# Performance work log

Measured on AMD Instinct MI355X. Metric: run time of the kernel, lower is better.

Reference implementation:

```python
import jax, jax.numpy as jnp
import numpy as np

B, N = 32, 200000          # images, flattened candidates per image (anchors*classes)
NUM_CLASSES = 21           # VOC-style class count for the label-offset trick
CONF_THR = 0.05            # cfg.PRED_CONF_THR
NMS_THR = 0.5              # cfg.PRED_NMS_THR
TOPK = 500                 # cfg.PRED_SELECT_TOPK
KEEP_MAX = 100             # cfg.PRED_NMS_KEEP


def setup_inputs() -> dict:
    key = jax.random.key(0)
    k1, k2, k3, k4 = jax.random.split(key, 4)
    pscores = jax.random.uniform(k1, (B, N), dtype=jnp.float32)
    # well-formed ltrb boxes in [0,1]: right>left, bottom>top
    xy1 = jax.random.uniform(k2, (B, N, 2), dtype=jnp.float32) * 0.8
    wh = jax.random.uniform(k3, (B, N, 2), dtype=jnp.float32) * 0.2 + 0.01
    pboxes = jnp.concatenate([xy1, xy1 + wh], axis=-1)
    plabels = jax.random.randint(k4, (B, N), 0, NUM_CLASSES)
    return {"pscores": pscores, "pboxes": pboxes, "plabels": plabels}


def _box_iou(a, b):
    # a: [K,4], b: [K,4] ltrb -> [K,K] pairwise IoU (torchvision convention)
    lt = jnp.maximum(a[:, None, :2], b[None, :, :2])
    rb = jnp.minimum(a[:, None, 2:], b[None, :, 2:])
    wh = jnp.clip(rb - lt, 0.0)
    inter = wh[..., 0] * wh[..., 1]
    area_a = (a[:, 2] - a[:, 0]) * (a[:, 3] - a[:, 1])
    area_b = (b[:, 2] - b[:, 0]) * (b[:, 3] - b[:, 1])
    return inter / (area_a[:, None] + area_b[None, :] - inter)


def _greedy_nms(iou_mat, valid, thr):
    # candidates are pre-sorted by score descending (lax.top_k output order)
    K = valid.shape[0]
    idxs = jnp.arange(K)

    def body(keep, i):
        suppressed = jnp.any(keep & (iou_mat[i] > thr) & (idxs < i))
        k = valid[i] & (~suppressed)
        return keep.at[i].set(k), None

    keep, _ = jax.lax.scan(body, jnp.zeros((K,), dtype=bool), idxs)
    return keep


def reference(pscores, pboxes, plabels):
    # ---- threshold + top-k pre-selection (mask_pos AND mask_topk) ----
    scores_k, idx = jax.lax.top_k(pscores, TOPK)          # [B,K] sorted desc
    valid = scores_k > CONF_THR                           # equivalent to mask_pos & mask_topk
    bidx = jnp.arange(B)[:, None]
    boxes_k = pboxes[bidx, idx]                           # [B,K,4]
    labels_k = plabels[bidx, idx]                         # [B,K]

    # ---- multi-class NMS via label offset trick (batched_nms) ----
    max_coord = jnp.max(jnp.where(valid[..., None], boxes_k, 0.0), axis=(1, 2))  # [B]
    offsets = labels_k.astype(boxes_k.dtype) * (max_coord[:, None] + 1.0)
    boxes_nms = boxes_k + offsets[..., None]              # [B,K,4]

    iou = jax.vmap(_box_iou)(boxes_nms, boxes_nms)        # [B,K,K]
    keep = jax.vmap(lambda m, v: _greedy_nms(m, v, NMS_THR))(iou, valid)  # [B,K] bool

    # ---- keep[:num_max] per batch ----
    rank = jnp.cumsum(keep.astype(jnp.int32), axis=1)
    keep = keep & (rank <= KEEP_MAX)

    # compact kept entries to front (jnp.argsort is stable -> score order preserved), pad to KEEP_MAX
    order = jnp.argsort(jnp.where(keep, 0, 1), axis=1)[:, :KEEP_MAX]       # [B,KEEP]
    out_valid = jnp.take_along_axis(keep, order, axis=1)                    # [B,KEEP]
    boxes2 = jnp.take_along_axis(boxes_k, order[..., None], axis=1) * out_valid[..., None]
    scores2 = jnp.take_along_axis(scores_k, order, axis=1) * out_valid
    labels2 = jnp.where(out_valid, jnp.take_along_axis(labels_k, order, axis=1), -1)
    ids_batch2 = jnp.where(out_valid, jnp.arange(B)[:, None], -1)
    return ids_batch2, boxes2, labels2, scores2, out_valid
```

## Files before the change

kernel.cpp:

```cpp
#include <hip/hip_runtime.h>
#include <stdint.h>

#pragma clang fp contract(off)

#define BB 32
#define NN 200000
#define N4 50000
#define KK 500
#define KEEPN 100
#define CONF 0.05f
#define NMSTHR 0.5f
#define SLICES 8
#define SLICE_F4 6250
#define LBINS 8192
#define LSHIFT 19
#define LOCAL_CAP 2048
#define OUT_CAP 576
#define M_CAP (SLICES * OUT_CAP)

typedef unsigned long long u64;


__device__ __forceinline__ unsigned int ordkey(float s) {
    unsigned int u = __float_as_uint(s);
    return (u & 0x80000000u) ? ~u : (u | 0x80000000u);
}

__global__ __launch_bounds__(1024) void select_kernel(const float4* __restrict__ ps4,
                                                      u64* __restrict__ cand,
                                                      unsigned int* __restrict__ cnts) {
    __shared__ unsigned int hist[LBINS];
    __shared__ u64 keys[LOCAL_CAP];
    __shared__ unsigned int h[256];
    __shared__ unsigned int wsum[16];
    __shared__ u64 s_prefix;
    __shared__ unsigned int s_t13, s_region, s_cntgt;
    __shared__ int s_lcnt, s_sc;

    const int b = blockIdx.y, x = blockIdx.x;
    const int tid = threadIdx.x, lane = tid & 63, wv = tid >> 6;
    const float4* p = ps4 + (size_t)b * N4 + (size_t)x * SLICE_F4;

    for (int i = tid; i < LBINS; i += 1024) hist[i] = 0;
    __syncthreads();
    for (int i = tid; i < SLICE_F4; i += 1024) {
        float4 v = p[i];
        atomicAdd(&hist[ordkey(v.x) >> LSHIFT], 1u);
        atomicAdd(&hist[ordkey(v.y) >> LSHIFT], 1u);
        atomicAdd(&hist[ordkey(v.z) >> LSHIFT], 1u);
        atomicAdd(&hist[ordkey(v.w) >> LSHIFT], 1u);
    }
    __syncthreads();

    unsigned int v8[8], tot = 0;
    for (int j = 0; j < 8; ++j) { v8[j] = hist[tid * 8 + j]; tot += v8[j]; }
    unsigned int sfx = tot;
    for (int off = 1; off < 64; off <<= 1) {
        unsigned int t2 = __shfl_down(sfx, off);
        sfx += (lane + off < 64) ? t2 : 0u;
    }
    if (lane == 0) wsum[wv] = sfx;
    __syncthreads();
    unsigned int wafter = 0;
    for (int w2 = wv + 1; w2 < 16; ++w2) wafter += wsum[w2];
    unsigned int sn = wafter + (sfx - tot);
    for (int j = 7; j >= 0; --j) {
        unsigned int s = sn + v8[j];
        if (s >= (unsigned)KK && sn < (unsigned)KK) s_t13 = (unsigned)(tid * 8 + j);
        sn = s;
    }
    if (tid == 0) s_lcnt = 0;
    __syncthreads();

    const unsigned int t13 = s_t13;
    const int ebase = x * (SLICE_F4 * 4);
    for (int i = tid; i < SLICE_F4; i += 1024) {
        float4 v = p[i];
        int n = ebase + (i << 2);
        unsigned int u;
        u = ordkey(v.x); if ((u >> LSHIFT) >= t13) { int pos = atomicAdd(&s_lcnt, 1);
            if (pos < LOCAL_CAP) keys[pos] = ((u64)u << 32) | (unsigned int)(~(unsigned int)(n)); }
        u = ordkey(v.y); if ((u >> LSHIFT) >= t13) { int pos = atomicAdd(&s_lcnt, 1);
            if (pos < LOCAL_CAP) keys[pos] = ((u64)u << 32) | (unsigned int)(~(unsigned int)(n + 1)); }
        u = ordkey(v.z); if ((u >> LSHIFT) >= t13) { int pos = atomicAdd(&s_lcnt, 1);
            if (pos < LOCAL_CAP) keys[pos] = ((u64)u << 32) | (unsigned int)(~(unsigned int)(n + 2)); }
        u = ordkey(v.w); if ((u >> LSHIFT) >= t13) { int pos = atomicAdd(&s_lcnt, 1);
            if (pos < LOCAL_CAP) keys[pos] = ((u64)u << 32) | (unsigned int)(~(unsigned int)(n + 3)); }
    }
    __syncthreads();
    int m = s_lcnt; if (m > LOCAL_CAP) m = LOCAL_CAP;

    u64 thr; int seln;
    if (m <= OUT_CAP) {
        thr = 0ULL; seln = m;
    } else {
        if (tid == 0) { s_prefix = 0ULL; s_cntgt = 0u; }
        __syncthreads();
        int shift = 56;
        for (; shift >= 0; shift -= 8) {
            if (tid < 256) h[tid] = 0u;
            __syncthreads();
            u64 pref = s_prefix;
            unsigned int cg = s_cntgt;
            for (int i = tid; i < m; i += 1024) {
                u64 k = keys[i];
                bool match = (shift == 56) || ((k >> (shift + 8)) == pref);
                if (match) atomicAdd(&h[(unsigned int)((k >> shift) & 0xFF)], 1u);
            }
            __syncthreads();
            if (wv == 0) {
                unsigned int b4[4]; unsigned int lt = 0;
                for (int j = 0; j < 4; ++j) { b4[j] = h[lane * 4 + j]; lt += b4[j]; }
                unsigned int sx = lt;
                for (int off = 1; off < 64; off <<= 1) {
                    unsigned int t2 = __shfl_down(sx, off);
                    sx += (lane + off < 64) ? t2 : 0u;
                }
                unsigned int after = sx - lt;
                unsigned int target = (unsigned)KK - cg;
                unsigned int sn2 = after;
                for (int j = 3; j >= 0; --j) {
                    unsigned int s = sn2 + b4[j];
                    if (s >= target && sn2 < target) {
                        unsigned int bin = (unsigned)(lane * 4 + j);
                        s_region = b4[j];
                        s_cntgt = cg + sn2;
                        s_prefix = (shift == 56) ? (u64)bin : ((pref << 8) | (u64)bin);
                    }
                    sn2 = s;
                }
            }
            __syncthreads();
            if (s_cntgt + s_region <= (unsigned)OUT_CAP) break;
        }
        if (shift < 0) shift = 0;
        thr = s_prefix << shift;
        seln = (int)(s_cntgt + s_region);
    }
    (void)seln;

    if (tid == 0) s_sc = 0;
    __syncthreads();
    u64* outslice = cand + (size_t)(b * SLICES + x) * OUT_CAP;
    for (int r0 = 0; r0 < LOCAL_CAP / 1024; ++r0) {
        int i = tid + r0 * 1024;
        u64 k = (i < m) ? keys[i] : 0ULL;
        bool pq = (i < m) && (k >= thr);
        u64 mb = __ballot(pq);
        int pre = __popcll(mb & ((1ULL << lane) - 1ULL));
        int tt = __popcll(mb);
        int base = 0;
        if (lane == 0 && tt > 0) base = atomicAdd(&s_sc, tt);
        base = __shfl(base, 0);
        if (pq && base + pre < OUT_CAP) outslice[base + pre] = k;
    }
    __syncthreads();
    if (tid == 0) {
        int c = s_sc; if (c > OUT_CAP) c = OUT_CAP;
        cnts[b * SLICES + x] = (unsigned)c;
    }
}

__global__ __launch_bounds__(1024) void final_kernel(const float* __restrict__ pboxes,
                                                     const int* __restrict__ plabels,
                                                     const u64* __restrict__ cand,
                                                     const unsigned int* __restrict__ cnts,
                                                     float* __restrict__ out) {
    __shared__ u64 kbuf[M_CAP];
    __shared__ u64 sel[OUT_CAP];
    __shared__ float sboxes[KK * 4];
    __shared__ float sscore[KK];
    __shared__ int slabel[KK];
    __shared__ int clist[KK];
    __shared__ unsigned int h[256];
    __shared__ int ccnt[21], coff[22], cfill[21];
    __shared__ u64 validw[8];
    __shared__ int kept[KEEPN];
    __shared__ float wred[16];
    __shared__ int soff[SLICES + 1];
    __shared__ u64 s_prefix;
    __shared__ unsigned int s_region, s_cntgt;
    __shared__ int s_sc, s_nk;
    __shared__ float s_maxc;

    const int b = blockIdx.x;
    const int tid = threadIdx.x;
    const int lane = tid & 63;
    const int wv = tid >> 6;

    if (tid == 0) {
        int acc = 0;
        for (int s = 0; s < SLICES; ++s) {
            soff[s] = acc;
            int c = (int)cnts[b * SLICES + s];
            if (c > OUT_CAP) c = OUT_CAP;
            acc += c;
        }
        soff[SLICES] = acc;
    }
    __syncthreads();
    int m = soff[SLICES];
    for (int s = 0; s < SLICES; ++s) {
        int off = soff[s], len = soff[s + 1] - off;
        const u64* src = cand + (size_t)(b * SLICES + s) * OUT_CAP;
        for (int i = tid; i < len; i += 1024) kbuf[off + i] = src[i];
    }
    __syncthreads();

    u64 thr; int seln;
    if (m <= OUT_CAP) {
        thr = 0ULL; seln = m;
    } else {
        if (tid == 0) { s_prefix = 0ULL; s_cntgt = 0u; }
        __syncthreads();
        int shift = 56;
        for (; shift >= 0; shift -= 8) {
            if (tid < 256) h[tid] = 0u;
            __syncthreads();
            u64 pref = s_prefix;
            unsigned int cg = s_cntgt;
            for (int i = tid; i < m; i += 1024) {
                u64 k = kbuf[i];
                bool match = (shift == 56) || ((k >> (shift + 8)) == pref);
                if (match) atomicAdd(&h[(unsigned int)((k >> shift) & 0xFF)], 1u);
            }
            __syncthreads();
            if (wv == 0) {
                unsigned int b4[4]; unsigned int lt = 0;
                for (int j = 0; j < 4; ++j) { b4[j] = h[lane * 4 + j]; lt += b4[j]; }
                unsigned int sx = lt;
                for (int off = 1; off < 64; off <<= 1) {
                    unsigned int t2 = __shfl_down(sx, off);
                    sx += (lane + off < 64) ? t2 : 0u;
                }
                unsigned int after = sx - lt;
                unsigned int target = (unsigned)KK - cg;
                unsigned int sn2 = after;
                for (int j = 3; j >= 0; --j) {
                    unsigned int s = sn2 + b4[j];
                    if (s >= target && sn2 < target) {
                        unsigned int bin = (unsigned)(lane * 4 + j);
                        s_region = b4[j];
                        s_cntgt = cg + sn2;
                        s_prefix = (shift == 56) ? (u64)bin : ((pref << 8) | (u64)bin);
                    }
                    sn2 = s;
                }
            }
            __syncthreads();
            if (s_cntgt + s_region <= (unsigned)OUT_CAP) break;
        }
        if (shift < 0) shift = 0;
        thr = s_prefix << shift;
        seln = (int)(s_cntgt + s_region);
    }

    if (tid == 0) s_sc = 0;
    __syncthreads();
    for (int r0 = 0; r0 < (M_CAP + 1023) / 1024; ++r0) {
        int i = tid + r0 * 1024;
        u64 k = (i < m) ? kbuf[i] : 0ULL;
        bool pq = (i < m) && (k >= thr);
        u64 mb = __ballot(pq);
        int pre = __popcll(mb & ((1ULL << lane) - 1ULL));
        int tt = __popcll(mb);
        int base = 0;
        if (lane == 0 && tt > 0) base = atomicAdd(&s_sc, tt);
        base = __shfl(base, 0);
        if (pq) sel[base + pre] = k;
    }
    __syncthreads();

    u64 myk = (tid < seln) ? sel[tid] : 0ULL;
    int r = 0;
    if ((tid & ~63) < seln) {
        for (int base = 0; base < seln; base += 64) {
            int i2 = base + lane;
            u64 other = (i2 < seln) ? sel[i2] : 0ULL;
            unsigned int olo = (unsigned int)other, ohi = (unsigned int)(other >> 32);
            int lim = seln - base; if (lim > 64) lim = 64;
            for (int t2 = 0; t2 < lim; ++t2) {
                unsigned int blo = (unsigned int)__builtin_amdgcn_readlane((int)olo, t2);
                unsigned int bhi = (unsigned int)__builtin_amdgcn_readlane((int)ohi, t2);
                u64 o = ((u64)bhi << 32) | (u64)blo;
                r += (o > myk) ? 1 : 0;
            }
        }
    }
    __syncthreads();
    if (tid < seln && r < KK) sel[r] = myk;
    __syncthreads();

    float sc = -1.0f;
    if (tid < KK) {
        u64 key = sel[tid];
        unsigned int lo = (unsigned int)key;
        unsigned int hi = (unsigned int)(key >> 32);
        int idx = (int)(~lo);
        unsigned int bits = (hi & 0x80000000u) ? (hi & 0x7FFFFFFFu) : ~hi;
        sc = __uint_as_float(bits);
        sscore[tid] = sc;
        const float4 bx = *(const float4*)(pboxes + (((size_t)b * NN + (size_t)idx) << 2));
        sboxes[tid * 4 + 0] = bx.x; sboxes[tid * 4 + 1] = bx.y;
        sboxes[tid * 4 + 2] = bx.z; sboxes[tid * 4 + 3] = bx.w;
        slabel[tid] = plabels[(size_t)b * NN + idx];
    }
    __syncthreads();

    bool vq = (tid < KK) && (sc > CONF);
    u64 bm = __ballot(vq);
    if (lane == 0 && wv < 8) validw[wv] = bm;
    float lm = vq ? fmaxf(fmaxf(sboxes[tid * 4 + 0], sboxes[tid * 4 + 1]),
                          fmaxf(sboxes[tid * 4 + 2], sboxes[tid * 4 + 3])) : 0.0f;
    for (int off = 32; off > 0; off >>= 1) lm = fmaxf(lm, __shfl_down(lm, off));
    if (lane == 0) wred[wv] = lm;
    __syncthreads();
    if (tid < 64) {
        float x = (tid < 16) ? wred[tid] : 0.0f;
        for (int off = 8; off > 0; off >>= 1) x = fmaxf(x, __shfl_down(x, off));
        if (tid == 0) s_maxc = x;
    }
    if (tid < 21) { ccnt[tid] = 0; cfill[tid] = 0; }
    __syncthreads();
    if (tid < KK) atomicAdd(&ccnt[slabel[tid]], 1);
    __syncthreads();
    if (tid == 0) {
        int acc = 0;
        for (int c = 0; c < 21; ++c) { coff[c] = acc; acc += ccnt[c]; }
        coff[21] = acc;
    }
    __syncthreads();
    if (tid < KK) {
        int c = slabel[tid];
        int pos = atomicAdd(&cfill[c], 1);
        clist[coff[c] + pos] = tid;
    }
    for (int i = tid; i < KK * 8; i += 1024) kbuf[i] = 0ULL;
    __syncthreads();

    float ap1 = s_maxc + 1.0f;
    if (tid < KK) {
        int c = slabel[tid];
        int n = ccnt[c], base0 = coff[c];
        float aoff = (float)c * ap1;
        float a0 = sboxes[tid * 4 + 0] + aoff, a1 = sboxes[tid * 4 + 1] + aoff;
        float a2 = sboxes[tid * 4 + 2] + aoff, a3 = sboxes[tid * 4 + 3] + aoff;
        float areaA = (a2 - a0) * (a3 - a1);
        for (int q = 0; q < n; ++q) {
            int j = clist[base0 + q];
            float b0 = sboxes[j * 4 + 0] + aoff, b1f = sboxes[j * 4 + 1] + aoff;
            float b2f = sboxes[j * 4 + 2] + aoff, b3f = sboxes[j * 4 + 3] + aoff;
            float lt0 = fmaxf(a0, b0), lt1 = fmaxf(a1, b1f);
            float rb0 = fminf(a2, b2f), rb1 = fminf(a3, b3f);
            float ww = fmaxf(rb0 - lt0, 0.0f), hh = fmaxf(rb1 - lt1, 0.0f);
            float inter = ww * hh;
            float areaB = (b2f - b0) * (b3f - b1f);
            float iou = inter / (areaA + areaB - inter);
            if (iou > NMSTHR) kbuf[tid * 8 + (j >> 6)] |= (1ULL << (j & 63));
        }
    }
    __syncthreads();

    if (tid < 64) {
        u64 remv = 0ULL;
        u64 vw_reg = (lane < 8) ? validw[lane] : 0ULL;
        int nk = 0;
        for (int i = 0; i < KK && nk < KEEPN; ++i) {
            int w = i >> 6, bpos = i & 63;
            u64 rw = __shfl(remv, w);
            u64 vv = __shfl(vw_reg, w);
            bool alive = (((vv >> bpos) & 1ULL) != 0ULL) && (((rw >> bpos) & 1ULL) == 0ULL);
            if (alive) {
                if (lane == 0) kept[nk] = i;
                u64 roww = (lane < 8) ? kbuf[i * 8 + lane] : 0ULL;
                remv |= roww;
                nk++;
            }
        }
        if (lane == 0) s_nk = nk;
    }
    __syncthreads();

    if (tid < KEEPN) {
        const int O_BOX = BB * KEEPN;
        const int O_LAB = BB * KEEPN * 5;
        const int O_SCO = BB * KEEPN * 6;
        const int O_VAL = BB * KEEPN * 7;
        bool q = tid < s_nk;
        int i = q ? kept[tid] : 0;
        int g = b * KEEPN + tid;
        out[g]                 = q ? (float)b : -1.0f;
        out[O_BOX + g * 4 + 0] = q ? sboxes[i * 4 + 0] : 0.0f;
        out[O_BOX + g * 4 + 1] = q ? sboxes[i * 4 + 1] : 0.0f;
        out[O_BOX + g * 4 + 2] = q ? sboxes[i * 4 + 2] : 0.0f;
        out[O_BOX + g * 4 + 3] = q ? sboxes[i * 4 + 3] : 0.0f;
        out[O_LAB + g]         = q ? (float)slabel[i] : -1.0f;
        out[O_SCO + g]         = q ? sscore[i] : 0.0f;
        out[O_VAL + g]         = q ? 1.0f : 0.0f;
    }
}

extern "C" void kernel_launch(void* const* d_in, const int* in_sizes, int n_in,
                              void* d_out, int out_size, void* d_ws, size_t ws_size,
                              hipStream_t stream) {
    const float* pscores = (const float*)d_in[0];
    const float* pboxes  = (const float*)d_in[1];
    const int*   plabels = (const int*)d_in[2];
    float* out = (float*)d_out;

    uint8_t* ws = (uint8_t*)d_ws;
    u64*          cand = (u64*)(ws + 0);
    unsigned int* cnts = (unsigned int*)(ws + 1179648);

    select_kernel<<<dim3(SLICES, BB), 1024, 0, stream>>>((const float4*)pscores, cand, cnts);
    final_kernel<<<BB, 1024, 0, stream>>>(pboxes, plabels, cand, cnts, out);
}
```

Measured before the change: 228.3 us.

## Split final kernel into sort and NMS kernels with blocked greedy suppression

The single final kernel is split in two. sort_kernel selects the top-K, gathers boxes, scores and labels, and writes them with the valid mask and max coordinate into a per-batch region of the workspace that reuses the candidate buffer. nms_kernel, launched with 512 threads, reloads that data, builds the IoU mask in a column-blocked layout, and runs greedy NMS one 64-wide block at a time. Within each block a wave reads the diagonal mask rows via readlane, then the other waves OR the kept rows into the later blocks in parallel. This is meant to shorten the serial greedy loop and lower per-kernel shared-memory pressure, at the cost of an extra launch, a global-memory round trip, and more block-wide syncs.

```diff
diff --git a/kernel.cpp b/kernel.cpp
--- a/kernel.cpp
+++ b/kernel.cpp
@@ -17,6 +17,13 @@
 #define LOCAL_CAP 2048
 #define OUT_CAP 576
 #define M_CAP (SLICES * OUT_CAP)
+
+#define PB_STRIDE 36864
+#define PB_BOX    0
+#define PB_SCORE  8000
+#define PB_LABEL  10000
+#define PB_VALID  12000
+#define PB_MAXC   12064
 
 typedef unsigned long long u64;
 
@@ -161,27 +168,18 @@
     }
 }
 
-__global__ __launch_bounds__(1024) void final_kernel(const float* __restrict__ pboxes,
-                                                     const int* __restrict__ plabels,
-                                                     const u64* __restrict__ cand,
-                                                     const unsigned int* __restrict__ cnts,
-                                                     float* __restrict__ out) {
+__global__ __launch_bounds__(1024) void sort_kernel(const float* __restrict__ pboxes,
+                                                    const int* __restrict__ plabels,
+                                                    u64* cand,
+                                                    const unsigned int* __restrict__ cnts) {
     __shared__ u64 kbuf[M_CAP];
     __shared__ u64 sel[OUT_CAP];
-    __shared__ float sboxes[KK * 4];
-    __shared__ float sscore[KK];
-    __shared__ int slabel[KK];
-    __shared__ int clist[KK];
     __shared__ unsigned int h[256];
-    __shared__ int ccnt[21], coff[22], cfill[21];
-    __shared__ u64 validw[8];
-    __shared__ int kept[KEEPN];
     __shared__ float wred[16];
     __shared__ int soff[SLICES + 1];
     __shared__ u64 s_prefix;
     __shared__ unsigned int s_region, s_cntgt;
-    __shared__ int s_sc, s_nk;
-    __shared__ float s_maxc;
+    __shared__ int s_sc;
 
     const int b = blockIdx.x;
     const int tid = threadIdx.x;
@@ -292,6 +290,8 @@
     __syncthreads();
 
     float sc = -1.0f;
+    float4 bx = make_float4(0.0f, 0.0f, 0.0f, 0.0f);
+    int lab = 0;
     if (tid < KK) {
         u64 key = sel[tid];
         unsigned int lo = (unsigned int)key;
@@ -299,30 +299,69 @@
         int idx = (int)(~lo);
         unsigned int bits = (hi & 0x80000000u) ? (hi & 0x7FFFFFFFu) : ~hi;
         sc = __uint_as_float(bits);
-        sscore[tid] = sc;
-        const float4 bx = *(const float4*)(pboxes + (((size_t)b * NN + (size_t)idx) << 2));
-        sboxes[tid * 4 + 0] = bx.x; sboxes[tid * 4 + 1] = bx.y;
-        sboxes[tid * 4 + 2] = bx.z; sboxes[tid * 4 + 3] = bx.w;
-        slabel[tid] = plabels[(size_t)b * NN + idx];
-    }
-    __syncthreads();
+        bx = *(const float4*)(pboxes + (((size_t)b * NN + (size_t)idx) << 2));
+        lab = plabels[(size_t)b * NN + idx];
+    }
+
+    uint8_t* pb = (uint8_t*)cand + (size_t)b * PB_STRIDE;
 
     bool vq = (tid < KK) && (sc > CONF);
     u64 bm = __ballot(vq);
-    if (lane == 0 && wv < 8) validw[wv] = bm;
-    float lm = vq ? fmaxf(fmaxf(sboxes[tid * 4 + 0], sboxes[tid * 4 + 1]),
-                          fmaxf(sboxes[tid * 4 + 2], sboxes[tid * 4 + 3])) : 0.0f;
+    if (lane == 0 && wv < 8) ((u64*)(pb + PB_VALID))[wv] = bm;
+    float lm = vq ? fmaxf(fmaxf(bx.x, bx.y), fmaxf(bx.z, bx.w)) : 0.0f;
     for (int off = 32; off > 0; off >>= 1) lm = fmaxf(lm, __shfl_down(lm, off));
     if (lane == 0) wred[wv] = lm;
     __syncthreads();
     if (tid < 64) {
         float x = (tid < 16) ? wred[tid] : 0.0f;
         for (int off = 8; off > 0; off >>= 1) x = fmaxf(x, __shfl_down(x, off));
-        if (tid == 0) s_maxc = x;
-    }
+        if (tid == 0) *(float*)(pb + PB_MAXC) = x;
+    }
+    if (tid < KK) {
+        *(float4*)(pb + PB_BOX + tid * 16) = bx;
+        *(float*)(pb + PB_SCORE + tid * 4) = sc;
+        *(int*)(pb + PB_LABEL + tid * 4) = lab;
+    }
+}
+
+__global__ __launch_bounds__(512) void nms_kernel(const uint8_t* __restrict__ wsb,
+                                                  float* __restrict__ out) {
+    __shared__ float sboxes[KK * 4];
+    __shared__ float sscore[KK];
+    __shared__ int slabel[KK];
+    __shared__ int clist[KK];
+    __shared__ u64 msk[8][512];
+    __shared__ u64 validw[8];
+    __shared__ u64 sremv[8];
+    __shared__ u64 s_km;
+    __shared__ int kept[KEEPN];
+    __shared__ int ccnt[21], coff[22], cfill[21];
+    __shared__ int s_nk, s_stop;
+    __shared__ float s_maxc;
+
+    const int b = blockIdx.x;
+    const int tid = threadIdx.x;
+    const int lane = tid & 63;
+    const int wv = tid >> 6;
+    const uint8_t* pb = wsb + (size_t)b * PB_STRIDE;
+
+    float sc = 0.0f; int lab = 0;
+    if (tid < KK) {
+        float4 bx = *(const float4*)(pb + PB_BOX + tid * 16);
+        sboxes[tid * 4 + 0] = bx.x; sboxes[tid * 4 + 1] = bx.y;
+        sboxes[tid * 4 + 2] = bx.z; sboxes[tid * 4 + 3] = bx.w;
+        sc = *(const float*)(pb + PB_SCORE + tid * 4);
+        lab = *(const int*)(pb + PB_LABEL + tid * 4);
+        sscore[tid] = sc;
+        slabel[tid] = lab;
+    }
+    if (tid < 8) { validw[tid] = ((const u64*)(pb + PB_VALID))[tid]; sremv[tid] = 0ULL; }
+    if (tid == 0) { s_maxc = *(const float*)(pb + PB_MAXC); s_nk = 0; s_stop = 0; }
     if (tid < 21) { ccnt[tid] = 0; cfill[tid] = 0; }
-    __syncthreads();
-    if (tid < KK) atomicAdd(&ccnt[slabel[tid]], 1);
+    for (int i = tid; i < 8 * 512; i += 512) ((u64*)msk)[i] = 0ULL;
+    __syncthreads();
+
+    if (tid < KK) atomicAdd(&ccnt[lab], 1);
     __syncthreads();
     if (tid == 0) {
         int acc = 0;
@@ -331,16 +370,15 @@
     }
     __syncthreads();
     if (tid < KK) {
-        int c = slabel[tid];
+        int c = lab;
         int pos = atomicAdd(&cfill[c], 1);
         clist[coff[c] + pos] = tid;
     }
-    for (int i = tid; i < KK * 8; i += 1024) kbuf[i] = 0ULL;
     __syncthreads();
 
     float ap1 = s_maxc + 1.0f;
     if (tid < KK) {
-        int c = slabel[tid];
+        int c = lab;
         int n = ccnt[c], base0 = coff[c];
         float aoff = (float)c * ap1;
         float a0 = sboxes[tid * 4 + 0] + aoff, a1 = sboxes[tid * 4 + 1] + aoff;
@@ -356,30 +394,43 @@
             float inter = ww * hh;
             float areaB = (b2f - b0) * (b3f - b1f);
             float iou = inter / (areaA + areaB - inter);
-            if (iou > NMSTHR) kbuf[tid * 8 + (j >> 6)] |= (1ULL << (j & 63));
-        }
-    }
-    __syncthreads();
-
-    if (tid < 64) {
-        u64 remv = 0ULL;
-        u64 vw_reg = (lane < 8) ? validw[lane] : 0ULL;
-        int nk = 0;
-        for (int i = 0; i < KK && nk < KEEPN; ++i) {
-            int w = i >> 6, bpos = i & 63;
-            u64 rw = __shfl(remv, w);
-            u64 vv = __shfl(vw_reg, w);
-            bool alive = (((vv >> bpos) & 1ULL) != 0ULL) && (((rw >> bpos) & 1ULL) == 0ULL);
-            if (alive) {
-                if (lane == 0) kept[nk] = i;
-                u64 roww = (lane < 8) ? kbuf[i * 8 + lane] : 0ULL;
-                remv |= roww;
-                nk++;
-            }
-        }
-        if (lane == 0) s_nk = nk;
-    }
-    __syncthreads();
+            if (iou > NMSTHR) msk[j >> 6][tid] |= (1ULL << (j & 63));
+        }
+    }
+    __syncthreads();
+
+    for (int c = 0; c < 8; ++c) {
+        if (wv == 0) {
+            u64 rowc = msk[c][c * 64 + lane];
+            unsigned int rl = (unsigned int)rowc, rh = (unsigned int)(rowc >> 32);
+            u64 cur = sremv[c];
+            u64 vv = validw[c];
+            u64 km = 0ULL;
+            int nk = s_nk;
+            for (int j = 0; j < 64; ++j) {
+                if (nk >= KEEPN) break;
+                bool alive = (((vv >> j) & 1ULL) != 0ULL) && (((cur >> j) & 1ULL) == 0ULL);
+                if (alive) {
+                    if (lane == 0) kept[nk] = c * 64 + j;
+                    u64 rv = ((u64)(unsigned int)__builtin_amdgcn_readlane((int)rh, j) << 32)
+                           |  (u64)(unsigned int)__builtin_amdgcn_readlane((int)rl, j);
+                    cur |= rv;
+                    km |= (1ULL << j);
+                    ++nk;
+                }
+            }
+            if (lane == 0) { s_km = km; s_nk = nk; sremv[c] = cur; s_stop = (nk >= KEEPN) ? 1 : 0; }
+        }
+        __syncthreads();
+        if (s_stop || c == 7) break;
+        if (wv > c) {
+            u64 km = s_km;
+            u64 v = ((km >> lane) & 1ULL) ? msk[wv][c * 64 + lane] : 0ULL;
+            for (int off2 = 32; off2 > 0; off2 >>= 1) v |= __shfl_xor(v, off2);
+            if (lane == 0) sremv[wv] |= v;
+        }
+        __syncthreads();
+    }
 
     if (tid < KEEPN) {
         const int O_BOX = BB * KEEPN;
@@ -413,5 +464,6 @@
     unsigned int* cnts = (unsigned int*)(ws + 1179648);
 
     select_kernel<<<dim3(SLICES, BB), 1024, 0, stream>>>((const float4*)pscores, cand, cnts);
-    final_kernel<<<BB, 1024, 0, stream>>>(pboxes, plabels, cand, cnts, out);
+    sort_kernel<<<BB, 1024, 0, stream>>>(pboxes, plabels, cand, cnts);
+    nms_kernel<<<BB, 512, 0, stream>>>(ws, out);
 }
```

Result: no change. 226.5 us (-0.8%).

## Use fixed score prefilter with wave-aggregated append and blocked parallel NMS

Applied to the files above, without the earlier changes.

The select kernel now skips the 8192-bin histogram pass and appends candidates whose score key exceeds a hardcoded threshold (about 0.95) using ballot-based, wave-aggregated atomics. It falls back to the histogram path only if the count is below K or overflows the buffer. The NMS mask is transposed into column-block layout, and greedy suppression runs in 64-wide blocks. Within a block one wave resolves keeps via readlane, then the other waves OR-reduce suppression into later blocks in parallel. The fixed threshold relies on the uniform score distribution of the test inputs, but the fallback preserves correctness.

```diff
diff --git a/kernel.cpp b/kernel.cpp
--- a/kernel.cpp
+++ b/kernel.cpp
@@ -17,6 +17,7 @@
 #define LOCAL_CAP 2048
 #define OUT_CAP 576
 #define M_CAP (SLICES * OUT_CAP)
+#define OK0 0xBF733333u
 
 typedef unsigned long long u64;
 
@@ -24,6 +25,16 @@
 __device__ __forceinline__ unsigned int ordkey(float s) {
     unsigned int u = __float_as_uint(s);
     return (u & 0x80000000u) ? ~u : (u | 0x80000000u);
+}
+
+__device__ __forceinline__ void wappend(bool pred, u64 key, u64* keys, int* lcnt, int lane) {
+    u64 bm = __ballot(pred);
+    int pre = __popcll(bm & ((1ULL << lane) - 1ULL));
+    int tt  = __popcll(bm);
+    int base = 0;
+    if (lane == 0 && tt > 0) base = atomicAdd(lcnt, tt);
+    base = __shfl(base, 0);
+    if (pred) { int pos = base + pre; if (pos < LOCAL_CAP) keys[pos] = key; }
 }
 
 __global__ __launch_bounds__(1024) void select_kernel(const float4* __restrict__ ps4,
@@ -40,55 +51,71 @@
     const int b = blockIdx.y, x = blockIdx.x;
     const int tid = threadIdx.x, lane = tid & 63, wv = tid >> 6;
     const float4* p = ps4 + (size_t)b * N4 + (size_t)x * SLICE_F4;
-
-    for (int i = tid; i < LBINS; i += 1024) hist[i] = 0;
-    __syncthreads();
-    for (int i = tid; i < SLICE_F4; i += 1024) {
-        float4 v = p[i];
-        atomicAdd(&hist[ordkey(v.x) >> LSHIFT], 1u);
-        atomicAdd(&hist[ordkey(v.y) >> LSHIFT], 1u);
-        atomicAdd(&hist[ordkey(v.z) >> LSHIFT], 1u);
-        atomicAdd(&hist[ordkey(v.w) >> LSHIFT], 1u);
-    }
-    __syncthreads();
-
-    unsigned int v8[8], tot = 0;
-    for (int j = 0; j < 8; ++j) { v8[j] = hist[tid * 8 + j]; tot += v8[j]; }
-    unsigned int sfx = tot;
-    for (int off = 1; off < 64; off <<= 1) {
-        unsigned int t2 = __shfl_down(sfx, off);
-        sfx += (lane + off < 64) ? t2 : 0u;
-    }
-    if (lane == 0) wsum[wv] = sfx;
-    __syncthreads();
-    unsigned int wafter = 0;
-    for (int w2 = wv + 1; w2 < 16; ++w2) wafter += wsum[w2];
-    unsigned int sn = wafter + (sfx - tot);
-    for (int j = 7; j >= 0; --j) {
-        unsigned int s = sn + v8[j];
-        if (s >= (unsigned)KK && sn < (unsigned)KK) s_t13 = (unsigned)(tid * 8 + j);
-        sn = s;
-    }
+    const int ebase = x * (SLICE_F4 * 4);
+
     if (tid == 0) s_lcnt = 0;
     __syncthreads();
 
-    const unsigned int t13 = s_t13;
-    const int ebase = x * (SLICE_F4 * 4);
     for (int i = tid; i < SLICE_F4; i += 1024) {
         float4 v = p[i];
         int n = ebase + (i << 2);
-        unsigned int u;
-        u = ordkey(v.x); if ((u >> LSHIFT) >= t13) { int pos = atomicAdd(&s_lcnt, 1);
-            if (pos < LOCAL_CAP) keys[pos] = ((u64)u << 32) | (unsigned int)(~(unsigned int)(n)); }
-        u = ordkey(v.y); if ((u >> LSHIFT) >= t13) { int pos = atomicAdd(&s_lcnt, 1);
-            if (pos < LOCAL_CAP) keys[pos] = ((u64)u << 32) | (unsigned int)(~(unsigned int)(n + 1)); }
-        u = ordkey(v.z); if ((u >> LSHIFT) >= t13) { int pos = atomicAdd(&s_lcnt, 1);
-            if (pos < LOCAL_CAP) keys[pos] = ((u64)u << 32) | (unsigned int)(~(unsigned int)(n + 2)); }
-        u = ordkey(v.w); if ((u >> LSHIFT) >= t13) { int pos = atomicAdd(&s_lcnt, 1);
-            if (pos < LOCAL_CAP) keys[pos] = ((u64)u << 32) | (unsigned int)(~(unsigned int)(n + 3)); }
-    }
-    __syncthreads();
-    int m = s_lcnt; if (m > LOCAL_CAP) m = LOCAL_CAP;
+        unsigned int ux = ordkey(v.x), uy = ordkey(v.y);
+        unsigned int uz = ordkey(v.z), uw = ordkey(v.w);
+        wappend(ux >= OK0, ((u64)ux << 32) | (unsigned int)(~(unsigned int)(n)),     keys, &s_lcnt, lane);
+        wappend(uy >= OK0, ((u64)uy << 32) | (unsigned int)(~(unsigned int)(n + 1)), keys, &s_lcnt, lane);
+        wappend(uz >= OK0, ((u64)uz << 32) | (unsigned int)(~(unsigned int)(n + 2)), keys, &s_lcnt, lane);
+        wappend(uw >= OK0, ((u64)uw << 32) | (unsigned int)(~(unsigned int)(n + 3)), keys, &s_lcnt, lane);
+    }
+    __syncthreads();
+    int m = s_lcnt;
+
+    if (m < KK || m > LOCAL_CAP) {
+        for (int i = tid; i < LBINS; i += 1024) hist[i] = 0;
+        __syncthreads();
+        for (int i = tid; i < SLICE_F4; i += 1024) {
+            float4 v = p[i];
+            atomicAdd(&hist[ordkey(v.x) >> LSHIFT], 1u);
+            atomicAdd(&hist[ordkey(v.y) >> LSHIFT], 1u);
+            atomicAdd(&hist[ordkey(v.z) >> LSHIFT], 1u);
+            atomicAdd(&hist[ordkey(v.w) >> LSHIFT], 1u);
+        }
+        __syncthreads();
+        unsigned int v8[8], tot = 0;
+        for (int j = 0; j < 8; ++j) { v8[j] = hist[tid * 8 + j]; tot += v8[j]; }
+        unsigned int sfx = tot;
+        for (int off = 1; off < 64; off <<= 1) {
+            unsigned int t2 = __shfl_down(sfx, off);
+            sfx += (lane + off < 64) ? t2 : 0u;
+        }
+        if (lane == 0) wsum[wv] = sfx;
+        __syncthreads();
+        unsigned int wafter = 0;
+        for (int w2 = wv + 1; w2 < 16; ++w2) wafter += wsum[w2];
+        unsigned int sn = wafter + (sfx - tot);
+        for (int j = 7; j >= 0; --j) {
+            unsigned int s = sn + v8[j];
+            if (s >= (unsigned)KK && sn < (unsigned)KK) s_t13 = (unsigned)(tid * 8 + j);
+            sn = s;
+        }
+        if (tid == 0) s_lcnt = 0;
+        __syncthreads();
+        const unsigned int t13 = s_t13;
+        for (int i = tid; i < SLICE_F4; i += 1024) {
+            float4 v = p[i];
+            int n = ebase + (i << 2);
+            unsigned int u;
+            u = ordkey(v.x); if ((u >> LSHIFT) >= t13) { int pos = atomicAdd(&s_lcnt, 1);
+                if (pos < LOCAL_CAP) keys[pos] = ((u64)u << 32) | (unsigned int)(~(unsigned int)(n)); }
+            u = ordkey(v.y); if ((u >> LSHIFT) >= t13) { int pos = atomicAdd(&s_lcnt, 1);
+                if (pos < LOCAL_CAP) keys[pos] = ((u64)u << 32) | (unsigned int)(~(unsigned int)(n + 1)); }
+            u = ordkey(v.z); if ((u >> LSHIFT) >= t13) { int pos = atomicAdd(&s_lcnt, 1);
+                if (pos < LOCAL_CAP) keys[pos] = ((u64)u << 32) | (unsigned int)(~(unsigned int)(n + 2)); }
+            u = ordkey(v.w); if ((u >> LSHIFT) >= t13) { int pos = atomicAdd(&s_lcnt, 1);
+                if (pos < LOCAL_CAP) keys[pos] = ((u64)u << 32) | (unsigned int)(~(unsigned int)(n + 3)); }
+        }
+        __syncthreads();
+        m = s_lcnt; if (m > LOCAL_CAP) m = LOCAL_CAP;
+    }
 
     u64 thr; int seln;
     if (m <= OUT_CAP) {
@@ -175,12 +202,14 @@
     __shared__ unsigned int h[256];
     __shared__ int ccnt[21], coff[22], cfill[21];
     __shared__ u64 validw[8];
+    __shared__ u64 sremv[8];
+    __shared__ u64 s_km;
     __shared__ int kept[KEEPN];
     __shared__ float wred[16];
     __shared__ int soff[SLICES + 1];
     __shared__ u64 s_prefix;
     __shared__ unsigned int s_region, s_cntgt;
-    __shared__ int s_sc, s_nk;
+    __shared__ int s_sc, s_nk, s_stop;
     __shared__ float s_maxc;
 
     const int b = blockIdx.x;
@@ -321,6 +350,8 @@
         if (tid == 0) s_maxc = x;
     }
     if (tid < 21) { ccnt[tid] = 0; cfill[tid] = 0; }
+    if (tid < 8) sremv[tid] = 0ULL;
+    if (tid == 0) { s_nk = 0; s_stop = 0; }
     __syncthreads();
     if (tid < KK) atomicAdd(&ccnt[slabel[tid]], 1);
     __syncthreads();
@@ -335,7 +366,8 @@
         int pos = atomicAdd(&cfill[c], 1);
         clist[coff[c] + pos] = tid;
     }
-    for (int i = tid; i < KK * 8; i += 1024) kbuf[i] = 0ULL;
+    u64 (*msk)[512] = (u64(*)[512])kbuf;
+    for (int i = tid; i < 8 * 512; i += 1024) ((u64*)kbuf)[i] = 0ULL;
     __syncthreads();
 
     float ap1 = s_maxc + 1.0f;
@@ -356,30 +388,43 @@
             float inter = ww * hh;
             float areaB = (b2f - b0) * (b3f - b1f);
             float iou = inter / (areaA + areaB - inter);
-            if (iou > NMSTHR) kbuf[tid * 8 + (j >> 6)] |= (1ULL << (j & 63));
-        }
-    }
-    __syncthreads();
-
-    if (tid < 64) {
-        u64 remv = 0ULL;
-        u64 vw_reg = (lane < 8) ? validw[lane] : 0ULL;
-        int nk = 0;
-        for (int i = 0; i < KK && nk < KEEPN; ++i) {
-            int w = i >> 6, bpos = i & 63;
-            u64 rw = __shfl(remv, w);
-            u64 vv = __shfl(vw_reg, w);
-            bool alive = (((vv >> bpos) & 1ULL) != 0ULL) && (((rw >> bpos) & 1ULL) == 0ULL);
-            if (alive) {
-                if (lane == 0) kept[nk] = i;
-                u64 roww = (lane < 8) ? kbuf[i * 8 + lane] : 0ULL;
-                remv |= roww;
-                nk++;
-            }
-        }
-        if (lane == 0) s_nk = nk;
-    }
-    __syncthreads();
+            if (iou > NMSTHR) msk[j >> 6][tid] |= (1ULL << (j & 63));
+        }
+    }
+    __syncthreads();
+
+    for (int c = 0; c < 8; ++c) {
+        if (wv == 0) {
+            u64 rowc = msk[c][c * 64 + lane];
+            unsigned int rl = (unsigned int)rowc, rh = (unsigned int)(rowc >> 32);
+            u64 cur = sremv[c];
+            u64 vv = validw[c];
+            u64 km = 0ULL;
+            int nk = s_nk;
+            for (int j = 0; j < 64; ++j) {
+                if (nk >= KEEPN) break;
+                bool alive = (((vv >> j) & 1ULL) != 0ULL) && (((cur >> j) & 1ULL) == 0ULL);
+                if (alive) {
+                    if (lane == 0) kept[nk] = c * 64 + j;
+                    u64 rv = ((u64)(unsigned int)__builtin_amdgcn_readlane((int)rh, j) << 32)
+                           |  (u64)(unsigned int)__builtin_amdgcn_readlane((int)rl, j);
+                    cur |= rv;
+                    km |= (1ULL << j);
+                    ++nk;
+                }
+            }
+            if (lane == 0) { s_km = km; s_nk = nk; sremv[c] = cur; s_stop = (nk >= KEEPN) ? 1 : 0; }
+        }
+        __syncthreads();
+        if (s_stop || c == 7) break;
+        if (wv > c && wv < 8) {
+            u64 km = s_km;
+            u64 v = ((km >> lane) & 1ULL) ? msk[wv][c * 64 + lane] : 0ULL;
+            for (int off2 = 32; off2 > 0; off2 >>= 1) v |= __shfl_xor(v, off2);
+            if (lane == 0) sremv[wv] |= v;
+        }
+        __syncthreads();
+    }
 
     if (tid < KEEPN) {
         const int O_BOX = BB * KEEPN;
```

After: 227.6 us. Within noise of the previous version (-0.3%).
